# Kernel optimization log

Measured on AMD Instinct MI355X. Metric: run time of the kernel, lower is better.

## Reference

```python
import jax, jax.numpy as jnp
import numpy as np
import math

N_HEADS = 8

def _head_dirs():
    # 8 trigrams = corners of {-1,+1}^3, L2-normalized -> each row / sqrt(3)
    t = np.array([[ (i >> 2 & 1) * 2 - 1, (i >> 1 & 1) * 2 - 1, (i & 1) * 2 - 1]
                  for i in range(8)], dtype=np.float32)
    return jnp.asarray(t / np.sqrt(3.0, dtype=np.float32))

def setup_inputs() -> dict:
    key = jax.random.key(0)
    k1, k2, k3, k4 = jax.random.split(key, 4)
    B, T, C = 2, 2048, 1024
    x = jax.random.normal(k1, (B, T, C), dtype=jnp.float32)
    w_qkv = jax.random.normal(k2, (C, 3 * C), dtype=jnp.float32) * (1.0 / math.sqrt(C))
    w_out = jax.random.normal(k3, (C, C), dtype=jnp.float32) * (1.0 / math.sqrt(C))
    head_scales = jax.random.normal(k4, (N_HEADS,), dtype=jnp.float32) * 0.1
    return {"x": x, "w_qkv": w_qkv, "w_out": w_out, "head_scales": head_scales}

def reference(x, w_qkv, w_out, head_scales):
    B, T, C = x.shape
    H = N_HEADS
    hd = C // H
    scale = 1.0 / math.sqrt(hd)
    dirs = _head_dirs()  # [H,3], fixed buffer

    qkv = (x @ w_qkv).reshape(B, T, 3, H, hd)
    q = jnp.transpose(qkv[:, :, 0], (0, 2, 1, 3))  # [B,H,T,hd]
    k = jnp.transpose(qkv[:, :, 1], (0, 2, 1, 3))
    v = jnp.transpose(qkv[:, :, 2], (0, 2, 1, 3))

    scores = jnp.einsum('bhqd,bhkd->bhqk', q, k) * scale  # [B,H,T,T]
    causal = jnp.tril(jnp.ones((T, T), dtype=bool))
    scores = jnp.where(causal[None, None], scores, -jnp.inf)

    # rank-1 geometric (trigram) bias on first 3 dims of q,k
    q_proj = jnp.einsum('bhtd,hd->bht', q[..., :3], dirs)  # [B,H,T]
    k_proj = jnp.einsum('bhtd,hd->bht', k[..., :3], dirs)
    geo = q_proj[..., :, None] * k_proj[..., None, :]       # [B,H,T,T]
    scores = scores + head_scales[None, :, None, None] * geo

    attn = jax.nn.softmax(scores, axis=-1)
    out = jnp.einsum('bhqk,bhkd->bqhd', attn, v).reshape(B, T, C)
    return out @ w_out
```

## Files before the change

### kernel.cpp

```cpp
#include <hip/hip_runtime.h>
#include <hip/hip_bf16.h>
#include <cstdint>
#include <cstddef>


namespace {
constexpr int kB = 2, kT = 2048, kC = 1024, kHD = 128;
constexpr int kM = kB * kT;
constexpr int kN3 = 3 * kC;
constexpr float kScale = 0.08838834764831845f;
constexpr float kInvS3 = 0.57735026918962576f;
constexpr float kL2E  = 1.4426950408889634f;
}

typedef __bf16 bf16x8 __attribute__((ext_vector_type(8)));
typedef float f32x4 __attribute__((ext_vector_type(4)));
typedef unsigned short u16x8 __attribute__((ext_vector_type(8)));
typedef unsigned short u16x4 __attribute__((ext_vector_type(4)));
typedef unsigned int u32x4 __attribute__((ext_vector_type(4)));

__device__ __forceinline__ unsigned short f2b(float f) {
  return __builtin_bit_cast(unsigned short, (__bf16)f);
}
__device__ __forceinline__ float b2f(unsigned short u) {
  return (float)__builtin_bit_cast(__bf16, u);
}
__device__ __forceinline__ void gll16(const void* g, void* lds) {
  __builtin_amdgcn_global_load_lds(
      (const __attribute__((address_space(1))) unsigned int*)g,
      (__attribute__((address_space(3))) unsigned int*)lds, 16, 0, 0);
}
__device__ __forceinline__ bf16x8 ldsv(const unsigned short* p) {
  return __builtin_bit_cast(bf16x8, *(const u16x8*)p);
}

__global__ void k_cvt(const float* __restrict__ in, unsigned short* __restrict__ out, int n4) {
  int i = blockIdx.x * 256 + threadIdx.x;
  if (i >= n4) return;
  float4 v = ((const float4*)in)[i];
  u16x4 o = { f2b(v.x), f2b(v.y), f2b(v.z), f2b(v.w) };
  ((u16x4*)out)[i] = o;
}

__global__ void k_tc(const float* __restrict__ in, unsigned short* __restrict__ out,
                     int R, int Cin) {
  __shared__ float tile[64][65];
  const int t = threadIdx.x;
  const int r0 = blockIdx.y * 64, c0 = blockIdx.x * 64;
  const int tr = t >> 4, tc4 = (t & 15) * 4;
#pragma unroll
  for (int rr = 0; rr < 4; ++rr) {
    int r = tr + rr * 16;
    float4 v = *(const float4*)&in[(size_t)(r0 + r) * Cin + c0 + tc4];
    tile[r][tc4 + 0] = v.x; tile[r][tc4 + 1] = v.y;
    tile[r][tc4 + 2] = v.z; tile[r][tc4 + 3] = v.w;
  }
  __syncthreads();
#pragma unroll
  for (int rr = 0; rr < 4; ++rr) {
    int c = tr + rr * 16;
    u16x4 o = { f2b(tile[tc4 + 0][c]), f2b(tile[tc4 + 1][c]),
                f2b(tile[tc4 + 2][c]), f2b(tile[tc4 + 3][c]) };
    *(u16x4*)&out[(size_t)(c0 + c) * R + r0 + tc4] = o;
  }
}

__global__ __launch_bounds__(256, 2) void k_gemm(
    const unsigned short* __restrict__ A,
    const unsigned short* __restrict__ Bt,
    unsigned short* __restrict__ Cb,
    float* __restrict__ Cf,
    int M, int N, int K, int ldc) {
  __shared__ unsigned short sA[2][4096];
  __shared__ unsigned short sB[2][4096];
  const int t = threadIdx.x;
  const int lane = t & 63, wave = t >> 6;
  const int g = lane >> 4, c16 = lane & 15;
  const int wr = wave >> 1, wc = wave & 1;
  const int brow = blockIdx.x * 128, bcol = blockIdx.y * 128;
  const int NT = K >> 5;

  f32x4 acc[4][4];
#pragma unroll
  for (int m = 0; m < 4; ++m)
#pragma unroll
    for (int n = 0; n < 4; ++n) acc[m][n] = 0.f;

  auto stage = [&](int buf, int kt) {
    const int k0 = kt * 32;
#pragma unroll
    for (int is = 0; is < 2; ++is) {
      int row = is * 64 + (t >> 2);
      int gs = (t & 3) ^ (row & 3);
      gll16(&A[(size_t)(brow + row) * K + k0 + gs * 8], &sA[buf][is * 2048 + wave * 512]);
      gll16(&Bt[(size_t)(bcol + row) * K + k0 + gs * 8], &sB[buf][is * 2048 + wave * 512]);
    }
  };

  stage(0, 0);
  __syncthreads();
  for (int kt = 0; kt < NT; ++kt) {
    if (kt + 1 < NT) stage((kt + 1) & 1, kt + 1);
    const int buf = kt & 1;
    bf16x8 av[4], bv[4];
#pragma unroll
    for (int m = 0; m < 4; ++m) {
      int row = wr * 64 + m * 16 + c16;
      av[m] = ldsv(&sA[buf][row * 32 + (g ^ (row & 3)) * 8]);
    }
#pragma unroll
    for (int n = 0; n < 4; ++n) {
      int row = wc * 64 + n * 16 + c16;
      bv[n] = ldsv(&sB[buf][row * 32 + (g ^ (row & 3)) * 8]);
    }
    __builtin_amdgcn_s_setprio(1);
#pragma unroll
    for (int m = 0; m < 4; ++m)
#pragma unroll
      for (int n = 0; n < 4; ++n)
        acc[m][n] = __builtin_amdgcn_mfma_f32_16x16x32_bf16(av[m], bv[n], acc[m][n], 0, 0, 0);
    __builtin_amdgcn_s_setprio(0);
    __syncthreads();
  }

  const int orow = brow + wr * 64, ocol = bcol + wc * 64;
  if (Cb != nullptr) {
#pragma unroll
    for (int m = 0; m < 4; ++m)
#pragma unroll
      for (int n = 0; n < 4; ++n)
#pragma unroll
        for (int jj = 0; jj < 4; ++jj)
          Cb[(size_t)(orow + m * 16 + g * 4 + jj) * ldc + ocol + n * 16 + c16] =
              f2b(acc[m][n][jj]);
  } else {
#pragma unroll
    for (int m = 0; m < 4; ++m)
#pragma unroll
      for (int n = 0; n < 4; ++n)
#pragma unroll
        for (int jj = 0; jj < 4; ++jj)
          Cf[(size_t)(orow + m * 16 + g * 4 + jj) * ldc + ocol + n * 16 + c16] =
              acc[m][n][jj];
  }
}

__constant__ unsigned char kItem[32] = {
  60, 61, 40, 41, 62, 56, 57, 58, 52, 36, 37, 16, 53, 54, 48, 49,
   0,  4,  8, 21, 20, 25, 24, 12, 29, 28, 46, 45, 44, 50, 33, 32 };

__global__ __launch_bounds__(256, 2) void k_attn(
    const unsigned short* __restrict__ qkv,
    const float* __restrict__ head_scales,
    unsigned short* __restrict__ pO0,
    unsigned short* __restrict__ pO1,
    unsigned short* __restrict__ pO2,
    float2* __restrict__ pml) {
  __shared__ unsigned short sK[2][8192];
  __shared__ unsigned short sVt[2][128 * 72];
  __shared__ float sKp[2][64];

  const int t = threadIdx.x;
  const int lane = t & 63, wave = t >> 6;
  const int g = lane >> 4, c16 = lane & 15;
  const int bh = blockIdx.x;
  const int it = kItem[blockIdx.y];
  const int qt = it >> 2, c = it & 3;
  const int n = 2 * qt + 2;
  const int nc = (qt <= 4) ? 1 : (qt <= 10) ? 2 : 3;
  const int cbase = n / nc, crem = n % nc;
  const int t0 = c * cbase + (c < crem ? c : crem);
  const int t1 = t0 + cbase + (c < crem ? 1 : 0);

  const int b = bh >> 3, h = bh & 7;
  const float hs = head_scales[h];
  const float sx = (h & 4) ? 1.f : -1.f;
  const float sy = (h & 2) ? 1.f : -1.f;
  const float sz = (h & 1) ? 1.f : -1.f;

  const int q0w = qt * 128 + wave * 32;
  const size_t rowbase = (size_t)b * kT;

  bf16x8 aq[2][4];
  float qp[2];
#pragma unroll
  for (int m = 0; m < 2; ++m) {
    const unsigned short* qrow = &qkv[(rowbase + q0w + m * 16 + c16) * kN3 + h * kHD];
#pragma unroll
    for (int ks = 0; ks < 4; ++ks) aq[m][ks] = ldsv(qrow + ks * 32 + g * 8);
    qp[m] = hs * kInvS3 * (sx * b2f(qrow[0]) + sy * b2f(qrow[1]) + sz * b2f(qrow[2]));
  }

  float mrow[2] = { -__builtin_inff(), -__builtin_inff() };
  float lrow[2] = { 0.f, 0.f };
  f32x4 oacc[2][8];
#pragma unroll
  for (int m = 0; m < 2; ++m)
#pragma unroll
    for (int dn = 0; dn < 8; ++dn) oacc[m][dn] = 0.f;

  uint4 vr[4];
  uint2 kpr;

  auto stageK = [&](int jt, int buf) {
    const int j0 = jt * 64;
#pragma unroll
    for (int is = 0; is < 4; ++is) {
      int row = is * 16 + (t >> 4);
      int gp = t & 15;
      int gs = (gp & 8) | ((gp ^ (row & 7)) & 7);
      gll16(&qkv[(rowbase + j0 + row) * kN3 + kC + h * kHD + gs * 8],
            &sK[buf][is * 2048 + wave * 512]);
    }
  };
  auto loadV = [&](int jt) {
#pragma unroll
    for (int itr = 0; itr < 4; ++itr)
      vr[itr] = *(const uint4*)&qkv[(rowbase + jt * 64 + lane) * kN3 + 2 * kC + h * kHD
                                    + (itr * 4 + wave) * 8];
  };
  auto writeV = [&](int buf) {
    unsigned int* sVtw = (unsigned int*)&sVt[buf][0];
    const int odd = lane & 1, pr = lane >> 1;
#pragma unroll
    for (int itr = 0; itr < 4; ++itr) {
      const int dg = itr * 4 + wave;
      uint4 my = vr[itr];
      unsigned int nx = __shfl_xor(my.x, 1), ny = __shfl_xor(my.y, 1);
      unsigned int nz = __shfl_xor(my.z, 1), nw = __shfl_xor(my.w, 1);
      unsigned int m01 = odd ? my.z : my.x, m23 = odd ? my.w : my.y;
      unsigned int n01 = odd ? nz : nx,     n23 = odd ? nw : ny;
      const int eb = odd * 4;
      unsigned int me, ne, w;
      me = m01 & 0xffffu;  ne = n01 & 0xffffu;
      w = odd ? (ne | (me << 16)) : (me | (ne << 16));
      sVtw[(dg * 8 + eb + 0) * 36 + pr] = w;
      me = m01 >> 16;      ne = n01 >> 16;
      w = odd ? (ne | (me << 16)) : (me | (ne << 16));
      sVtw[(dg * 8 + eb + 1) * 36 + pr] = w;
      me = m23 & 0xffffu;  ne = n23 & 0xffffu;
      w = odd ? (ne | (me << 16)) : (me | (ne << 16));
      sVtw[(dg * 8 + eb + 2) * 36 + pr] = w;
      me = m23 >> 16;      ne = n23 >> 16;
      w = odd ? (ne | (me << 16)) : (me | (ne << 16));
      sVtw[(dg * 8 + eb + 3) * 36 + pr] = w;
    }
  };
  auto loadKp = [&](int jt) {
    if (wave == 0)
      kpr = *(const uint2*)&qkv[(rowbase + jt * 64 + lane) * kN3 + kC + h * kHD];
  };
  auto writeKp = [&](int buf) {
    if (wave == 0) {
      float e0 = b2f((unsigned short)(kpr.x & 0xffffu));
      float e1 = b2f((unsigned short)(kpr.x >> 16));
      float e2 = b2f((unsigned short)(kpr.y & 0xffffu));
      sKp[buf][lane] = kInvS3 * (sx * e0 + sy * e1 + sz * e2);
    }
  };

  stageK(t0, 0); loadV(t0); loadKp(t0);
  writeV(0); writeKp(0);
  __syncthreads();

  for (int jt = t0; jt < t1; ++jt) {
    const int buf = (jt - t0) & 1;
    const bool more = (jt + 1 < t1);
    if (more) { stageK(jt + 1, buf ^ 1); loadV(jt + 1); loadKp(jt + 1); }

    const int j0 = jt * 64;
    f32x4 s[2][4];
#pragma unroll
    for (int m = 0; m < 2; ++m)
#pragma unroll
      for (int nn = 0; nn < 4; ++nn) s[m][nn] = 0.f;
#pragma unroll
    for (int ks = 0; ks < 4; ++ks) {
      bf16x8 kb[4];
#pragma unroll
      for (int nn = 0; nn < 4; ++nn) {
        int gp = ks * 4 + g;
        int gp2 = (gp & 8) | ((gp ^ (c16 & 7)) & 7);
        kb[nn] = ldsv(&sK[buf][(nn * 16 + c16) * 128 + gp2 * 8]);
      }
      __builtin_amdgcn_s_setprio(1);
#pragma unroll
      for (int m = 0; m < 2; ++m)
#pragma unroll
        for (int nn = 0; nn < 4; ++nn)
          s[m][nn] = __builtin_amdgcn_mfma_f32_16x16x32_bf16(kb[nn], aq[m][ks], s[m][nn], 0, 0, 0);
      __builtin_amdgcn_s_setprio(0);
    }

    float kpv[4][4];
#pragma unroll
    for (int nn = 0; nn < 4; ++nn)
#pragma unroll
      for (int jj = 0; jj < 4; ++jj) kpv[nn][jj] = sKp[buf][nn * 16 + g * 4 + jj];

    const bool edge = (jt >= 2 * qt);
    unsigned int paf[2][2][4];
#pragma unroll
    for (int m = 0; m < 2; ++m) {
      const int qg = q0w + m * 16 + c16;
      float vmax = -__builtin_inff();
#pragma unroll
      for (int nn = 0; nn < 4; ++nn)
#pragma unroll
        for (int jj = 0; jj < 4; ++jj) {
          float xv = s[m][nn][jj] * kScale + qp[m] * kpv[nn][jj];
          if (edge) {
            int kvg = j0 + nn * 16 + g * 4 + jj;
            xv = (kvg <= qg) ? xv : -__builtin_inff();
          }
          s[m][nn][jj] = xv;
          vmax = fmaxf(vmax, xv);
        }
      vmax = fmaxf(vmax, __shfl_xor(vmax, 16, 64));
      vmax = fmaxf(vmax, __shfl_xor(vmax, 32, 64));

      if (__any(vmax > mrow[m])) {
        float mnew = fmaxf(mrow[m], vmax);
        float mc0 = fmaxf(mnew, -1e30f);
        float alpha = exp2f((mrow[m] - mc0) * kL2E);
        mrow[m] = mnew;
        lrow[m] *= alpha;
        float ao[4];
#pragma unroll
        for (int jj = 0; jj < 4; ++jj)
          ao[jj] = __shfl(alpha, (lane & 48) | (g * 4 + jj), 64);
#pragma unroll
        for (int dn = 0; dn < 8; ++dn)
#pragma unroll
          for (int jj = 0; jj < 4; ++jj) oacc[m][dn][jj] *= ao[jj];
      }

      unsigned int pk[4][2];
      {
        const float mc = fmaxf(mrow[m], -1e30f);
        float ls = 0.f;
#pragma unroll
        for (int nn = 0; nn < 4; ++nn) {
          float p0 = exp2f((s[m][nn][0] - mc) * kL2E);
          float p1 = exp2f((s[m][nn][1] - mc) * kL2E);
          float p2 = exp2f((s[m][nn][2] - mc) * kL2E);
          float p3 = exp2f((s[m][nn][3] - mc) * kL2E);
          ls += (p0 + p1) + (p2 + p3);
          pk[nn][0] = (unsigned)f2b(p0) | ((unsigned)f2b(p1) << 16);
          pk[nn][1] = (unsigned)f2b(p2) | ((unsigned)f2b(p3) << 16);
        }
        lrow[m] += ls;
      }
#pragma unroll
      for (int ks2 = 0; ks2 < 2; ++ks2)
#pragma unroll
        for (int w = 0; w < 4; ++w) {
          int src = c16 + (((lane >> 4) & 1) * 2 + (w >> 1)) * 16;
          int va  = __shfl((int)pk[2 * ks2][w & 1], src, 64);
          int vb_ = __shfl((int)pk[2 * ks2 + 1][w & 1], src, 64);
          paf[m][ks2][w] = (unsigned)((lane & 32) ? vb_ : va);
        }
    }

#pragma unroll
    for (int ks2 = 0; ks2 < 2; ++ks2) {
      bf16x8 pa0 = __builtin_bit_cast(bf16x8,
          (u32x4){paf[0][ks2][0], paf[0][ks2][1], paf[0][ks2][2], paf[0][ks2][3]});
      bf16x8 pa1 = __builtin_bit_cast(bf16x8,
          (u32x4){paf[1][ks2][0], paf[1][ks2][1], paf[1][ks2][2], paf[1][ks2][3]});
      __builtin_amdgcn_s_setprio(1);
#pragma unroll
      for (int dn = 0; dn < 8; ++dn) {
        bf16x8 vb = ldsv(&sVt[buf][(dn * 16 + c16) * 72 + ks2 * 32 + g * 8]);
        oacc[0][dn] = __builtin_amdgcn_mfma_f32_16x16x32_bf16(pa0, vb, oacc[0][dn], 0, 0, 0);
        oacc[1][dn] = __builtin_amdgcn_mfma_f32_16x16x32_bf16(pa1, vb, oacc[1][dn], 0, 0, 0);
      }
      __builtin_amdgcn_s_setprio(0);
    }

    if (more) { writeV(buf ^ 1); writeKp(buf ^ 1); }
    __syncthreads();
  }

  unsigned short* pout = (c == 0) ? pO0 : (c == 1) ? pO1 : pO2;
#pragma unroll
  for (int m = 0; m < 2; ++m) {
    float lt = lrow[m];
    lt += __shfl_xor(lt, 16, 64);
    lt += __shfl_xor(lt, 32, 64);
    if (g == 0) {
      int rowi = wave * 32 + m * 16 + c16;
      pml[c * 32768 + (bh * 16 + qt) * 128 + rowi] = make_float2(mrow[m], lt);
    }
#pragma unroll
    for (int dn = 0; dn < 8; ++dn)
#pragma unroll
      for (int jj = 0; jj < 4; ++jj) {
        int r = q0w + m * 16 + g * 4 + jj;
        pout[(rowbase + r) * kC + h * kHD + dn * 16 + c16] = f2b(oacc[m][dn][jj]);
      }
  }
}

__global__ void k_comb(unsigned short* __restrict__ p0,
                       const unsigned short* __restrict__ p1,
                       const unsigned short* __restrict__ p2,
                       const float2* __restrict__ pml) {
  const int bh = blockIdx.x, qt = blockIdx.y;
  const int t = threadIdx.x;
  const int row = t >> 1, half = t & 1;
  const int b = bh >> 3, h = bh & 7;
  const size_t base = ((size_t)b * kT + qt * 128 + row) * kC + h * kHD + half * 64;
  const int nc = (qt <= 4) ? 1 : (qt <= 10) ? 2 : 3;
  const int mli = (bh * 16 + qt) * 128 + row;
  float2 ml0 = pml[mli];
  float2 ml1 = make_float2(-1e30f, 0.f), ml2 = make_float2(-1e30f, 0.f);
  float mm = ml0.x;
  if (nc > 1) { ml1 = pml[32768 + mli]; mm = fmaxf(mm, ml1.x); }
  if (nc > 2) { ml2 = pml[65536 + mli]; mm = fmaxf(mm, ml2.x); }
  const float w0 = exp2f((ml0.x - mm) * kL2E);
  const float w1 = (nc > 1) ? exp2f((ml1.x - mm) * kL2E) : 0.f;
  const float w2 = (nc > 2) ? exp2f((ml2.x - mm) * kL2E) : 0.f;
  const float inv = 1.0f / (w0 * ml0.y + w1 * ml1.y + w2 * ml2.y);
#pragma unroll
  for (int i = 0; i < 8; ++i) {
    u16x8 o0 = *(const u16x8*)&p0[base + i * 8];
    u16x8 r;
    if (nc == 1) {
#pragma unroll
      for (int j = 0; j < 8; ++j) r[j] = f2b(b2f(o0[j]) * inv);
    } else if (nc == 2) {
      u16x8 o1 = *(const u16x8*)&p1[base + i * 8];
#pragma unroll
      for (int j = 0; j < 8; ++j)
        r[j] = f2b((w0 * b2f(o0[j]) + w1 * b2f(o1[j])) * inv);
    } else {
      u16x8 o1 = *(const u16x8*)&p1[base + i * 8];
      u16x8 o2 = *(const u16x8*)&p2[base + i * 8];
#pragma unroll
      for (int j = 0; j < 8; ++j)
        r[j] = f2b((w0 * b2f(o0[j]) + w1 * b2f(o1[j]) + w2 * b2f(o2[j])) * inv);
    }
    *(u16x8*)&p0[base + i * 8] = r;
  }
}

extern "C" void kernel_launch(void* const* d_in, const int* in_sizes, int n_in,
                              void* d_out, int out_size, void* d_ws, size_t ws_size,
                              hipStream_t stream) {
  const float* x    = (const float*)d_in[0];
  const float* wqkv = (const float*)d_in[1];
  const float* wout = (const float*)d_in[2];
  const float* hsc  = (const float*)d_in[3];
  char* ws = (char*)d_ws;
  unsigned short* xb    = (unsigned short*)(ws);
  unsigned short* wqkvT = (unsigned short*)(ws + 8388608);
  unsigned short* qkvb  = (unsigned short*)(ws + 16777216);
  unsigned short* attnb = (unsigned short*)(ws + 41943040);
  unsigned short* woutT = (unsigned short*)(ws);
  float2* pml = (float2*)d_out;
  float* out = (float*)d_out;

  k_cvt<<<dim3(4096), dim3(256), 0, stream>>>(x, xb, kM * kC / 4);
  k_tc<<<dim3(48, 16), dim3(256), 0, stream>>>(wqkv, wqkvT, kC, kN3);
  k_gemm<<<dim3(32, 24), dim3(256), 0, stream>>>(xb, wqkvT, qkvb, nullptr, kM, kN3, kC, kN3);
  k_attn<<<dim3(16, 32), dim3(256), 0, stream>>>(qkvb, hsc, attnb, xb, wqkvT, pml);
  k_comb<<<dim3(16, 16), dim3(256), 0, stream>>>(attnb, xb, wqkvT, pml);
  k_tc<<<dim3(16, 16), dim3(256), 0, stream>>>(wout, woutT, kC, kC);
  k_gemm<<<dim3(32, 8), dim3(256), 0, stream>>>(attnb, woutT, nullptr, out, kM, kC, kC, kC);
}
```

Baseline: 139.4 us.

## Single-buffer V tile, raise attention occupancy, and finer KV split scheduling

```diff
diff --git a/kernel.cpp b/kernel.cpp
--- a/kernel.cpp
+++ b/kernel.cpp
@@ -145,11 +145,19 @@
   }
 }
 
-__constant__ unsigned char kItem[32] = {
-  60, 61, 40, 41, 62, 56, 57, 58, 52, 36, 37, 16, 53, 54, 48, 49,
-   0,  4,  8, 21, 20, 25, 24, 12, 29, 28, 46, 45, 44, 50, 33, 32 };
-
-__global__ __launch_bounds__(256, 2) void k_attn(
+__constant__ unsigned char kItem[44] = {
+  60, 61,
+  62, 56, 57, 58, 52,
+  53, 54, 48, 49,
+  50, 44, 45, 46, 40,
+  41, 42, 36, 37,
+  38, 32, 33, 34, 28,
+  29, 30, 24, 25,
+  26, 20, 21, 22, 16,
+  17, 18, 12, 13, 8, 9,
+  14, 4, 5, 0 };
+
+__global__ __launch_bounds__(256, 3) void k_attn(
     const unsigned short* __restrict__ qkv,
     const float* __restrict__ head_scales,
     unsigned short* __restrict__ pO0,
@@ -157,7 +165,7 @@
     unsigned short* __restrict__ pO2,
     float2* __restrict__ pml) {
   __shared__ unsigned short sK[2][8192];
-  __shared__ unsigned short sVt[2][128 * 72];
+  __shared__ unsigned short sVt[128 * 72];
   __shared__ float sKp[2][64];
 
   const int t = threadIdx.x;
@@ -167,7 +175,7 @@
   const int it = kItem[blockIdx.y];
   const int qt = it >> 2, c = it & 3;
   const int n = 2 * qt + 2;
-  const int nc = (qt <= 4) ? 1 : (qt <= 10) ? 2 : 3;
+  const int nc = (qt == 0) ? 1 : (qt <= 2) ? 2 : 3;
   const int cbase = n / nc, crem = n % nc;
   const int t0 = c * cbase + (c < crem ? c : crem);
   const int t1 = t0 + cbase + (c < crem ? 1 : 0);
@@ -219,8 +227,8 @@
       vr[itr] = *(const uint4*)&qkv[(rowbase + jt * 64 + lane) * kN3 + 2 * kC + h * kHD
                                     + (itr * 4 + wave) * 8];
   };
-  auto writeV = [&](int buf) {
-    unsigned int* sVtw = (unsigned int*)&sVt[buf][0];
+  auto writeV = [&]() {
+    unsigned int* sVtw = (unsigned int*)&sVt[0];
     const int odd = lane & 1, pr = lane >> 1;
 #pragma unroll
     for (int itr = 0; itr < 4; ++itr) {
@@ -260,13 +268,13 @@
   };
 
   stageK(t0, 0); loadV(t0); loadKp(t0);
-  writeV(0); writeKp(0);
+  writeV(); writeKp(0);
   __syncthreads();
 
   for (int jt = t0; jt < t1; ++jt) {
-    const int buf = (jt - t0) & 1;
+    const int kbuf = (jt - t0) & 1;
     const bool more = (jt + 1 < t1);
-    if (more) { stageK(jt + 1, buf ^ 1); loadV(jt + 1); loadKp(jt + 1); }
+    if (more) { stageK(jt + 1, kbuf ^ 1); loadV(jt + 1); loadKp(jt + 1); }
 
     const int j0 = jt * 64;
     f32x4 s[2][4];
@@ -281,7 +289,7 @@
       for (int nn = 0; nn < 4; ++nn) {
         int gp = ks * 4 + g;
         int gp2 = (gp & 8) | ((gp ^ (c16 & 7)) & 7);
-        kb[nn] = ldsv(&sK[buf][(nn * 16 + c16) * 128 + gp2 * 8]);
+        kb[nn] = ldsv(&sK[kbuf][(nn * 16 + c16) * 128 + gp2 * 8]);
       }
       __builtin_amdgcn_s_setprio(1);
 #pragma unroll
@@ -296,7 +304,7 @@
 #pragma unroll
     for (int nn = 0; nn < 4; ++nn)
 #pragma unroll
-      for (int jj = 0; jj < 4; ++jj) kpv[nn][jj] = sKp[buf][nn * 16 + g * 4 + jj];
+      for (int jj = 0; jj < 4; ++jj) kpv[nn][jj] = sKp[kbuf][nn * 16 + g * 4 + jj];
 
     const bool edge = (jt >= 2 * qt);
     unsigned int paf[2][2][4];
@@ -319,10 +327,9 @@
       vmax = fmaxf(vmax, __shfl_xor(vmax, 16, 64));
       vmax = fmaxf(vmax, __shfl_xor(vmax, 32, 64));
 
-      if (__any(vmax > mrow[m])) {
+      if (__any(vmax > mrow[m] + 8.f)) {
         float mnew = fmaxf(mrow[m], vmax);
-        float mc0 = fmaxf(mnew, -1e30f);
-        float alpha = exp2f((mrow[m] - mc0) * kL2E);
+        float alpha = exp2f((mrow[m] - mnew) * kL2E);
         mrow[m] = mnew;
         lrow[m] *= alpha;
         float ao[4];
@@ -371,15 +378,18 @@
       __builtin_amdgcn_s_setprio(1);
 #pragma unroll
       for (int dn = 0; dn < 8; ++dn) {
-        bf16x8 vb = ldsv(&sVt[buf][(dn * 16 + c16) * 72 + ks2 * 32 + g * 8]);
+        bf16x8 vb = ldsv(&sVt[(dn * 16 + c16) * 72 + ks2 * 32 + g * 8]);
         oacc[0][dn] = __builtin_amdgcn_mfma_f32_16x16x32_bf16(pa0, vb, oacc[0][dn], 0, 0, 0);
         oacc[1][dn] = __builtin_amdgcn_mfma_f32_16x16x32_bf16(pa1, vb, oacc[1][dn], 0, 0, 0);
       }
       __builtin_amdgcn_s_setprio(0);
     }
 
-    if (more) { writeV(buf ^ 1); writeKp(buf ^ 1); }
-    __syncthreads();
+    if (more) {
+      __syncthreads();
+      writeV(); writeKp(kbuf ^ 1);
+      __syncthreads();
+    }
   }
 
   unsigned short* pout = (c == 0) ? pO0 : (c == 1) ? pO1 : pO2;
@@ -411,7 +421,7 @@
   const int row = t >> 1, half = t & 1;
   const int b = bh >> 3, h = bh & 7;
   const size_t base = ((size_t)b * kT + qt * 128 + row) * kC + h * kHD + half * 64;
-  const int nc = (qt <= 4) ? 1 : (qt <= 10) ? 2 : 3;
+  const int nc = (qt == 0) ? 1 : (qt <= 2) ? 2 : 3;
   const int mli = (bh * 16 + qt) * 128 + row;
   float2 ml0 = pml[mli];
   float2 ml1 = make_float2(-1e30f, 0.f), ml2 = make_float2(-1e30f, 0.f);
@@ -464,7 +474,7 @@
   k_cvt<<<dim3(4096), dim3(256), 0, stream>>>(x, xb, kM * kC / 4);
   k_tc<<<dim3(48, 16), dim3(256), 0, stream>>>(wqkv, wqkvT, kC, kN3);
   k_gemm<<<dim3(32, 24), dim3(256), 0, stream>>>(xb, wqkvT, qkvb, nullptr, kM, kN3, kC, kN3);
-  k_attn<<<dim3(16, 32), dim3(256), 0, stream>>>(qkvb, hsc, attnb, xb, wqkvT, pml);
+  k_attn<<<dim3(16, 44), dim3(256), 0, stream>>>(qkvb, hsc, attnb, xb, wqkvT, pml);
   k_comb<<<dim3(16, 16), dim3(256), 0, stream>>>(attnb, xb, wqkvT, pml);
   k_tc<<<dim3(16, 16), dim3(256), 0, stream>>>(wout, woutT, kC, kC);
   k_gemm<<<dim3(32, 8), dim3(256), 0, stream>>>(attnb, woutT, nullptr, out, kM, kC, kC, kC);
```

Result: slower. 234.7 us (+68.4%).
